# Performance work log

Measured on AMD Instinct MI355X. Metric: run time of the kernel, lower is better.

Reference implementation:

```python
import jax, jax.numpy as jnp
import numpy as np

TEMP = 0.025
BN_EPS = 1e-5


def _attention(a, W_in, b_in, g, beta, rm, rv, W_out, b_out):
    # a: (b, n1, n2, P, Q); 1x1 conv over the Q 'channel' dim, gate, softmax over P.
    m = a.mean(axis=3)                                   # (b,n1,n2,Q)
    t = jnp.einsum('bnmq,kq->bnmk', m, W_in) + b_in      # (b,n1,n2,K)
    t = jax.nn.relu((t - rm) / jnp.sqrt(rv + BN_EPS) * g + beta)
    t = jnp.einsum('bnmk,qk->bnmq', t, W_out) + b_out    # (b,n1,n2,Q)
    s = jnp.mean(a * t[:, :, :, None, :], axis=-1)       # (b,n1,n2,P)
    return jax.nn.softmax(s / TEMP, axis=-1) + 1.0


def _cam_forward(zf, xf, conv1_w, conv1_b, bn1_g, bn1_b, bn1_rm, bn1_rv,
                 conv2_w, conv2_b, conv3_w, conv3_b, bn3_g, bn3_b, bn3_rm, bn3_rv,
                 conv4_w, conv4_b):
    out1, out2 = [], []
    L = zf.shape[0]
    for l in range(L):  # small fixed loop over feature levels
        f1, f2 = zf[l], xf[l]
        b, c, h1, w1 = f1.shape
        h2, w2 = f2.shape[2], f2.shape[3]
        P, Q = h1 * w1, h2 * w2
        f1s = jnp.stack([f1.reshape(b, c, P)] * 2, axis=1)   # (b,2,c,P)
        f2s = jnp.stack([f2.reshape(b, c, Q)] * 2, axis=1)   # (b,2,c,Q)
        f1n = f1s / jnp.maximum(jnp.linalg.norm(f1s, axis=2, keepdims=True), 1e-12)
        f2n = f2s / jnp.maximum(jnp.linalg.norm(f2s, axis=2, keepdims=True), 1e-12)
        a1 = jnp.einsum('bncp,bmcq->bnmpq', f1n, f2n)        # (b,2,2,P,Q)
        att1 = _attention(a1, conv1_w, conv1_b, bn1_g, bn1_b, bn1_rm, bn1_rv,
                          conv2_w, conv2_b)                  # (b,2,2,P)
        att2 = _attention(a1.swapaxes(3, 4), conv3_w, conv3_b, bn3_g, bn3_b,
                          bn3_rm, bn3_rv, conv4_w, conv4_b)  # (b,2,2,Q)
        # mean over the (n1,n2)=(2,2) pair grid without materializing (b,2,2,c,HW)
        o1 = jnp.einsum('bncp,bnmp->bcp', f1s, att1) / 4.0
        o2 = jnp.einsum('bmcq,bnmq->bcq', f2s, att2) / 4.0
        out1.append(o1.reshape(b, c, h1, w1))
        out2.append(o2.reshape(b, c, h2, w2))
    return (jnp.stack(out1), jnp.stack(out2))


def setup_inputs() -> dict:
    key = jax.random.key(0)
    ks = jax.random.split(key, 12)
    L, B, C = 3, 32, 256
    inp = {
        'zf': jax.random.normal(ks[0], (L, B, C, 7, 7), jnp.float32),
        'xf': jax.random.normal(ks[1], (L, B, C, 31, 31), jnp.float32),
        'conv1_w': jax.random.normal(ks[2], (31, 961), jnp.float32) * np.sqrt(2.0 / 31),
        'conv1_b': jax.random.normal(ks[3], (31,), jnp.float32) * 0.05,
        'bn1_g': jax.random.uniform(ks[4], (31,), jnp.float32, 0.5, 1.5),
        'bn1_b': jax.random.normal(ks[5], (31,), jnp.float32) * 0.05,
        'bn1_rm': jnp.zeros((31,), jnp.float32),
        'bn1_rv': jnp.ones((31,), jnp.float32),
        'conv2_w': jax.random.normal(ks[6], (961, 31), jnp.float32) * np.sqrt(2.0 / 961),
        'conv2_b': jax.random.normal(ks[7], (961,), jnp.float32) * 0.05,
        'conv3_w': jax.random.normal(ks[8], (7, 49), jnp.float32) * np.sqrt(2.0 / 7),
        'conv3_b': jax.random.normal(ks[9], (7,), jnp.float32) * 0.05,
        'bn3_g': jax.random.uniform(ks[10], (7,), jnp.float32, 0.5, 1.5),
        'bn3_b': jax.random.normal(ks[11], (7,), jnp.float32) * 0.05,
        'bn3_rm': jnp.zeros((7,), jnp.float32),
        'bn3_rv': jnp.ones((7,), jnp.float32),
        'conv4_w': jax.random.normal(jax.random.fold_in(key, 100), (49, 7), jnp.float32) * np.sqrt(2.0 / 49),
        'conv4_b': jax.random.normal(jax.random.fold_in(key, 101), (49,), jnp.float32) * 0.05,
    }
    return inp


def reference(zf, xf, conv1_w, conv1_b, bn1_g, bn1_b, bn1_rm, bn1_rv,
              conv2_w, conv2_b, conv3_w, conv3_b, bn3_g, bn3_b, bn3_rm, bn3_rv,
              conv4_w, conv4_b):
    return _cam_forward(zf, xf, conv1_w, conv1_b, bn1_g, bn1_b, bn1_rm, bn1_rv,
                        conv2_w, conv2_b, conv3_w, conv3_b, bn3_g, bn3_b,
                        bn3_rm, bn3_rv, conv4_w, conv4_b)
```

## Files before the change

### kernel.cpp

```cpp
#include <hip/hip_runtime.h>
#include <math.h>

#define NLB 96
#define CC  256
#define PP  49
#define QQ  961
#define QP  1024
#define TEMP_INV 40.0f
#define BN_EPS 1e-5f

#define N1 (NLB*CC*PP)
#define N2 (NLB*CC*QQ)

typedef __attribute__((ext_vector_type(8))) short bf16x8;
typedef __attribute__((ext_vector_type(4))) float f32x4;
typedef __attribute__((ext_vector_type(8))) unsigned short ushort8;

__device__ inline unsigned short f2bf(float x) {
    unsigned int u = __float_as_uint(x);
    unsigned int r = (u + 0x7fffu + ((u >> 16) & 1u)) >> 16;
    return (unsigned short)r;
}

__global__ __launch_bounds__(256) void prep_z(
    const float* __restrict__ zf, unsigned short* __restrict__ f1T,
    float* __restrict__ inv1_ws, float* __restrict__ mrow_ws)
{
    const int lb = blockIdx.x;
    if (threadIdx.x < PP) mrow_ws[lb * PP + threadIdx.x] = 0.f;

    const float* __restrict__ f1 = zf + (size_t)lb * CC * PP;
    const int p  = threadIdx.x >> 2;
    const int qu = threadIdx.x & 3;
    const int c0 = qu * 64;
    float ss = 0.f;
    ushort8* dst = (ushort8*)(f1T + ((size_t)lb * 64 + p) * CC + c0);
#pragma unroll
    for (int s = 0; s < 8; ++s) {
        unsigned short tmp[8];
#pragma unroll
        for (int j = 0; j < 8; ++j) {
            const float v = (p < PP) ? f1[(size_t)(c0 + s * 8 + j) * PP + p] : 0.f;
            ss = fmaf(v, v, ss);
            tmp[j] = f2bf(v);
        }
        dst[s] = *(ushort8*)tmp;
    }
    ss += __shfl_xor(ss, 1, 64);
    ss += __shfl_xor(ss, 2, 64);
    if (qu == 0) inv1_ws[lb * 64 + p] = (p < PP) ? 1.0f / fmaxf(sqrtf(ss), 1e-12f) : 0.f;
}

__global__ __launch_bounds__(256) void prep_x(
    const float* __restrict__ xf, unsigned short* __restrict__ xT,
    float* __restrict__ inv2_ws)
{
    const int qt = blockIdx.x;
    const int lb = blockIdx.y;
    const int q0 = qt * 64;
    const float* __restrict__ f2 = xf + (size_t)lb * CC * QQ;

    __shared__ __align__(16) unsigned short tileB[64 * 264];
    __shared__ float ssP[4][64];

    const int tid  = threadIdx.x;
    const int lane = tid & 63;
    const int w    = tid >> 6;

    const int q  = q0 + lane;
    const bool qv = (q < QQ);
    float ss = 0.f;

    for (int i = 0; i < 8; ++i) {
        float r[8];
#pragma unroll
        for (int j = 0; j < 8; ++j) {
            const int c = (i * 8 + j) * 4 + w;
            r[j] = qv ? f2[(size_t)c * QQ + q] : 0.f;
        }
#pragma unroll
        for (int j = 0; j < 8; ++j) {
            const int c = (i * 8 + j) * 4 + w;
            ss = fmaf(r[j], r[j], ss);
            tileB[lane * 264 + c] = f2bf(r[j]);
        }
    }
    ssP[w][lane] = ss;
    __syncthreads();

    if (tid < 64) {
        const float t = ssP[0][tid] + ssP[1][tid] + ssP[2][tid] + ssP[3][tid];
        inv2_ws[lb * QP + q0 + tid] = 1.0f / fmaxf(sqrtf(t), 1e-12f);
    }

    unsigned short* __restrict__ dst = xT + (size_t)(lb * QP + q0) * CC;
#pragma unroll
    for (int j = 0; j < 8; ++j) {
        const int flat = (j * 256 + tid) * 8;
        const int qq = flat >> 8;
        const int cc = flat & 255;
        const ushort8 vv = *(const ushort8*)&tileB[qq * 264 + cc];
        *(ushort8*)&dst[flat] = vv;
    }
}

__global__ __launch_bounds__(256) void corr_mfma(
    const unsigned short* __restrict__ f1T, const unsigned short* __restrict__ xT,
    const float* __restrict__ inv1_ws, const float* __restrict__ inv2_ws,
    float* __restrict__ A_all, float* __restrict__ mcol_ws,
    float* __restrict__ mrow_ws)
{
    const int ng = blockIdx.x;
    const int lb = blockIdx.y;
    const int tid  = threadIdx.x;
    const int lane = tid & 63;
    const int wave = tid >> 6;
    const int g4   = lane >> 4;
    const int l15  = lane & 15;

    __shared__ __align__(16) unsigned short f1L[64 * 264];
    __shared__ float inv1L[64];

    for (int i = tid; i < 64 * 32; i += 256) {
        const int row = i >> 5, seg = i & 31;
        *(ushort8*)&f1L[row * 264 + seg * 8] =
            *(const ushort8*)&f1T[((size_t)lb * 64 + row) * CC + seg * 8];
    }
    if (tid < 64) inv1L[tid] = inv1_ws[lb * 64 + tid];
    __syncthreads();

    f32x4 acc[4][4];
#pragma unroll
    for (int i = 0; i < 4; ++i)
#pragma unroll
        for (int mt = 0; mt < 4; ++mt) acc[i][mt] = (f32x4)0.f;

    const unsigned short* __restrict__ xTb = xT + ((size_t)(lb * QP + ng * 256)) * CC;

#pragma unroll
    for (int kc = 0; kc < 4; ++kc) {
        bf16x8 af[4][2];
#pragma unroll
        for (int mt = 0; mt < 4; ++mt)
#pragma unroll
            for (int ks = 0; ks < 2; ++ks)
                af[mt][ks] = *(const bf16x8*)&f1L[(mt * 16 + l15) * 264 + kc * 64 + ks * 32 + g4 * 8];
#pragma unroll
        for (int i = 0; i < 4; ++i) {
            const int rowq = (4 * i + wave) * 16 + l15;
#pragma unroll
            for (int ks = 0; ks < 2; ++ks) {
                const bf16x8 bfr = *(const bf16x8*)&xTb[(size_t)rowq * CC + kc * 64 + ks * 32 + g4 * 8];
#pragma unroll
                for (int mt = 0; mt < 4; ++mt)
                    acc[i][mt] = __builtin_amdgcn_mfma_f32_16x16x32_bf16(af[mt][ks], bfr, acc[i][mt], 0, 0, 0);
            }
        }
    }

    float* __restrict__ Aout = A_all + (size_t)lb * PP * QQ;
#pragma unroll
    for (int i = 0; i < 4; ++i) {
        const int nt = 4 * i + wave;
        const int qg = ng * 256 + nt * 16 + l15;
        const bool qvv = (qg < QQ);
        const float iv2 = inv2_ws[lb * QP + qg];
        float vv[16];
        float cs = 0.f;
#pragma unroll
        for (int mt = 0; mt < 4; ++mt)
#pragma unroll
            for (int r = 0; r < 4; ++r) {
                const int p = mt * 16 + g4 * 4 + r;
                const float v = acc[i][mt][r] * inv1L[p] * iv2;
                vv[mt * 4 + r] = v;
                cs += v;
                if (p < PP && qvv) Aout[(size_t)p * QQ + qg] = v;
            }
        cs += __shfl_xor(cs, 16, 64);
        cs += __shfl_xor(cs, 32, 64);
        if ((lane < 16) && qvv) mcol_ws[lb * QQ + qg] = cs;
#pragma unroll
        for (int mt = 0; mt < 4; ++mt)
#pragma unroll
            for (int r = 0; r < 4; ++r) {
                const int p = mt * 16 + g4 * 4 + r;
                float s = vv[mt * 4 + r];
                s += __shfl_xor(s, 1, 64);
                s += __shfl_xor(s, 2, 64);
                s += __shfl_xor(s, 4, 64);
                s += __shfl_xor(s, 8, 64);
                if (((lane & 15) == 0) && p < PP) atomicAdd(&mrow_ws[lb * PP + p], s);
            }
    }
}

__global__ __launch_bounds__(512) void attn_kernel(
    const float* __restrict__ A_all,
    const float* __restrict__ mcol_ws, const float* __restrict__ mrow_ws,
    const float* __restrict__ W1, const float* __restrict__ b1,
    const float* __restrict__ g1, const float* __restrict__ bb1,
    const float* __restrict__ rm1, const float* __restrict__ rv1,
    const float* __restrict__ W2, const float* __restrict__ b2,
    const float* __restrict__ W3, const float* __restrict__ b3,
    const float* __restrict__ g3, const float* __restrict__ bb3,
    const float* __restrict__ rm3, const float* __restrict__ rv3,
    const float* __restrict__ W4, const float* __restrict__ b4,
    float* __restrict__ att1_ws, float* __restrict__ att2_ws)
{
    const int lb = blockIdx.x;
    const float* __restrict__ A = A_all + (size_t)lb * PP * QQ;
    const int tid  = threadIdx.x;
    const int lane = tid & 63;
    const int wv   = tid >> 6;

    __shared__ float mcolL[QQ];
    __shared__ float mrowL[PP];
    __shared__ float taL[31], tbL[7];
    __shared__ float t2aL[QQ], t2bL[PP];
    __shared__ float s2sL[QQ];
    __shared__ float s1L[PP];
    __shared__ float redM[8], redS[8];

    for (int q = tid; q < QQ; q += 512) mcolL[q] = mcol_ws[lb * QQ + q] * (1.0f / PP);
    if (tid < PP) mrowL[tid] = mrow_ws[lb * PP + tid] * (1.0f / QQ);
    __syncthreads();

    if (tid < 31 * 16) {
        const int k = tid >> 4, sub = tid & 15;
        float s = 0.f;
        for (int q = sub; q < QQ; q += 16) s = fmaf(mcolL[q], W1[k * QQ + q], s);
        s += __shfl_xor(s, 1, 64); s += __shfl_xor(s, 2, 64);
        s += __shfl_xor(s, 4, 64); s += __shfl_xor(s, 8, 64);
        if (sub == 0) {
            float t = s + b1[k];
            t = (t - rm1[k]) * rsqrtf(rv1[k] + BN_EPS) * g1[k] + bb1[k];
            taL[k] = fmaxf(t, 0.f);
        }
    }
    if (tid < 7 * 8) {
        const int k = tid >> 3, sub = tid & 7;
        float s = 0.f;
        for (int p = sub; p < PP; p += 8) s = fmaf(mrowL[p], W3[k * PP + p], s);
        s += __shfl_xor(s, 1, 64); s += __shfl_xor(s, 2, 64); s += __shfl_xor(s, 4, 64);
        if (sub == 0) {
            float t = s + b3[k];
            t = (t - rm3[k]) * rsqrtf(rv3[k] + BN_EPS) * g3[k] + bb3[k];
            tbL[k] = fmaxf(t, 0.f);
        }
    }
    __syncthreads();

    for (int q = tid; q < QQ; q += 512) {
        float s = b2[q];
#pragma unroll
        for (int k = 0; k < 31; ++k) s = fmaf(taL[k], W2[q * 31 + k], s);
        t2aL[q] = s;
    }
    if (tid < PP) {
        float s = b4[tid];
#pragma unroll
        for (int k = 0; k < 7; ++k) s = fmaf(tbL[k], W4[tid * 7 + k], s);
        t2bL[tid] = s;
    }
    __syncthreads();

    for (int q = tid; q < QQ; q += 512) {
        float s = 0.f;
#pragma unroll
        for (int p = 0; p < PP; ++p) s = fmaf(A[(size_t)p * QQ + q], t2bL[p], s);
        s2sL[q] = s * (1.0f / PP) * TEMP_INV;
    }
    for (int p = wv; p < PP; p += 8) {
        float s = 0.f;
        for (int q = lane; q < QQ; q += 64) s = fmaf(A[(size_t)p * QQ + q], t2aL[q], s);
        for (int off = 32; off > 0; off >>= 1) s += __shfl_xor(s, off, 64);
        if (lane == 0) s1L[p] = s * (1.0f / QQ) * TEMP_INV;
    }
    __syncthreads();

    if (wv == 0) {
        const float v = (lane < PP) ? s1L[lane] : -3.4e38f;
        float m = v;
        for (int off = 32; off > 0; off >>= 1) m = fmaxf(m, __shfl_xor(m, off, 64));
        const float e = (lane < PP) ? expf(v - m) : 0.f;
        float sum = e;
        for (int off = 32; off > 0; off >>= 1) sum += __shfl_xor(sum, off, 64);
        if (lane < PP) att1_ws[lb * PP + lane] = e / sum + 1.0f;
    }

    float lm = -3.4e38f;
    for (int q = tid; q < QQ; q += 512) lm = fmaxf(lm, s2sL[q]);
    for (int off = 32; off > 0; off >>= 1) lm = fmaxf(lm, __shfl_xor(lm, off, 64));
    if (lane == 0) redM[wv] = lm;
    __syncthreads();
    float gm = redM[0];
#pragma unroll
    for (int i = 1; i < 8; ++i) gm = fmaxf(gm, redM[i]);
    float ls = 0.f;
    for (int q = tid; q < QQ; q += 512) ls += expf(s2sL[q] - gm);
    for (int off = 32; off > 0; off >>= 1) ls += __shfl_xor(ls, off, 64);
    if (lane == 0) redS[wv] = ls;
    __syncthreads();
    float tot = 0.f;
#pragma unroll
    for (int i = 0; i < 8; ++i) tot += redS[i];
    const float rinv = 1.0f / tot;
    for (int q = tid; q < QQ; q += 512)
        att2_ws[lb * QQ + q] = expf(s2sL[q] - gm) * rinv + 1.0f;
}

template <int INNER>
__global__ __launch_bounds__(256) void scale_kernel(
    const float* __restrict__ in, const float* __restrict__ att,
    float* __restrict__ out, int n4)
{
    const int i = blockIdx.x * 256 + threadIdx.x;
    if (i >= n4) return;
    const float4 v = reinterpret_cast<const float4*>(in)[i];
    const float* vv = reinterpret_cast<const float*>(&v);
    float4 o;
    float* ov = reinterpret_cast<float*>(&o);
    const int g = i * 4;
#pragma unroll
    for (int j = 0; j < 4; ++j) {
        const int gg = g + j;
        const int lb = gg / (CC * INNER);
        const int x  = gg % INNER;
        ov[j] = vv[j] * att[lb * INNER + x];
    }
    reinterpret_cast<float4*>(out)[i] = o;
}

extern "C" void kernel_launch(void* const* d_in, const int* in_sizes, int n_in,
                              void* d_out, int out_size, void* d_ws, size_t ws_size,
                              hipStream_t stream)
{
    const float* zf  = (const float*)d_in[0];
    const float* xf  = (const float*)d_in[1];
    const float* W1  = (const float*)d_in[2];
    const float* b1  = (const float*)d_in[3];
    const float* g1  = (const float*)d_in[4];
    const float* bb1 = (const float*)d_in[5];
    const float* rm1 = (const float*)d_in[6];
    const float* rv1 = (const float*)d_in[7];
    const float* W2  = (const float*)d_in[8];
    const float* b2  = (const float*)d_in[9];
    const float* W3  = (const float*)d_in[10];
    const float* b3  = (const float*)d_in[11];
    const float* g3  = (const float*)d_in[12];
    const float* bb3 = (const float*)d_in[13];
    const float* rm3 = (const float*)d_in[14];
    const float* rv3 = (const float*)d_in[15];
    const float* W4  = (const float*)d_in[16];
    const float* b4  = (const float*)d_in[17];

    char* wsb = (char*)d_ws;
    unsigned short* xT  = (unsigned short*)wsb;
    unsigned short* f1T = xT + (size_t)NLB * QP * CC;
    float* fbase = (float*)(f1T + (size_t)NLB * 64 * CC);
    float* A     = fbase;
    float* att1  = A + (size_t)NLB * PP * QQ;
    float* att2  = att1 + (size_t)NLB * PP;
    float* mcol  = att2 + (size_t)NLB * QQ;
    float* mrow  = mcol + (size_t)NLB * QQ;
    float* inv1  = mrow + (size_t)NLB * PP;
    float* inv2  = inv1 + (size_t)NLB * 64;

    float* out1 = (float*)d_out;
    float* out2 = out1 + N1;

    prep_z<<<NLB, 256, 0, stream>>>(zf, f1T, inv1, mrow);
    dim3 gx(16, NLB);
    prep_x<<<gx, 256, 0, stream>>>(xf, xT, inv2);

    dim3 gcorr(4, NLB);
    corr_mfma<<<gcorr, 256, 0, stream>>>(f1T, xT, inv1, inv2, A, mcol, mrow);

    attn_kernel<<<NLB, 512, 0, stream>>>(A, mcol, mrow,
        W1, b1, g1, bb1, rm1, rv1, W2, b2,
        W3, b3, g3, bb3, rm3, rv3, W4, b4,
        att1, att2);

    const int n4_1 = N1 / 4;
    const int n4_2 = N2 / 4;
    scale_kernel<PP><<<(n4_1 + 255) / 256, 256, 0, stream>>>(zf, att1, out1, n4_1);
    scale_kernel<QQ><<<(n4_2 + 255) / 256, 256, 0, stream>>>(xf, att2, out2, n4_2);
}
```

Measured before the change: 149.1 us.

## Fuse x-feature bf16 conversion and norm into correlation MFMA kernel

Removes the separate prep_x kernel that transposed xf into a bf16 workspace and computed inverse norms. corr_mfma now reads fp32 xf directly in its natural channel-major layout, converts to bf16 in registers, and accumulates squared norms per column, reducing across lanes with shuffles. This drops a kernel launch and a full write+read of the transposed bf16 copy. In exchange each B-fragment load becomes eight strided scalar fp32 loads (stride QQ), though lanes read consecutive q, so the loads coalesce across the wavefront.

```diff
diff --git a/kernel.cpp b/kernel.cpp
--- a/kernel.cpp
+++ b/kernel.cpp
@@ -5,7 +5,6 @@
 #define CC  256
 #define PP  49
 #define QQ  961
-#define QP  1024
 #define TEMP_INV 40.0f
 #define BN_EPS 1e-5f
 
@@ -51,62 +50,9 @@
     if (qu == 0) inv1_ws[lb * 64 + p] = (p < PP) ? 1.0f / fmaxf(sqrtf(ss), 1e-12f) : 0.f;
 }
 
-__global__ __launch_bounds__(256) void prep_x(
-    const float* __restrict__ xf, unsigned short* __restrict__ xT,
-    float* __restrict__ inv2_ws)
-{
-    const int qt = blockIdx.x;
-    const int lb = blockIdx.y;
-    const int q0 = qt * 64;
-    const float* __restrict__ f2 = xf + (size_t)lb * CC * QQ;
-
-    __shared__ __align__(16) unsigned short tileB[64 * 264];
-    __shared__ float ssP[4][64];
-
-    const int tid  = threadIdx.x;
-    const int lane = tid & 63;
-    const int w    = tid >> 6;
-
-    const int q  = q0 + lane;
-    const bool qv = (q < QQ);
-    float ss = 0.f;
-
-    for (int i = 0; i < 8; ++i) {
-        float r[8];
-#pragma unroll
-        for (int j = 0; j < 8; ++j) {
-            const int c = (i * 8 + j) * 4 + w;
-            r[j] = qv ? f2[(size_t)c * QQ + q] : 0.f;
-        }
-#pragma unroll
-        for (int j = 0; j < 8; ++j) {
-            const int c = (i * 8 + j) * 4 + w;
-            ss = fmaf(r[j], r[j], ss);
-            tileB[lane * 264 + c] = f2bf(r[j]);
-        }
-    }
-    ssP[w][lane] = ss;
-    __syncthreads();
-
-    if (tid < 64) {
-        const float t = ssP[0][tid] + ssP[1][tid] + ssP[2][tid] + ssP[3][tid];
-        inv2_ws[lb * QP + q0 + tid] = 1.0f / fmaxf(sqrtf(t), 1e-12f);
-    }
-
-    unsigned short* __restrict__ dst = xT + (size_t)(lb * QP + q0) * CC;
-#pragma unroll
-    for (int j = 0; j < 8; ++j) {
-        const int flat = (j * 256 + tid) * 8;
-        const int qq = flat >> 8;
-        const int cc = flat & 255;
-        const ushort8 vv = *(const ushort8*)&tileB[qq * 264 + cc];
-        *(ushort8*)&dst[flat] = vv;
-    }
-}
-
 __global__ __launch_bounds__(256) void corr_mfma(
-    const unsigned short* __restrict__ f1T, const unsigned short* __restrict__ xT,
-    const float* __restrict__ inv1_ws, const float* __restrict__ inv2_ws,
+    const unsigned short* __restrict__ f1T, const float* __restrict__ xf,
+    const float* __restrict__ inv1_ws,
     float* __restrict__ A_all, float* __restrict__ mcol_ws,
     float* __restrict__ mrow_ws)
 {
@@ -118,6 +64,8 @@
     const int g4   = lane >> 4;
     const int l15  = lane & 15;
 
+    const float* __restrict__ f2 = xf + (size_t)lb * CC * QQ;
+
     __shared__ __align__(16) unsigned short f1L[64 * 264];
     __shared__ float inv1L[64];
 
@@ -135,7 +83,7 @@
 #pragma unroll
         for (int mt = 0; mt < 4; ++mt) acc[i][mt] = (f32x4)0.f;
 
-    const unsigned short* __restrict__ xTb = xT + ((size_t)(lb * QP + ng * 256)) * CC;
+    float ss2[4] = {0.f, 0.f, 0.f, 0.f};
 
 #pragma unroll
     for (int kc = 0; kc < 4; ++kc) {
@@ -147,10 +95,22 @@
                 af[mt][ks] = *(const bf16x8*)&f1L[(mt * 16 + l15) * 264 + kc * 64 + ks * 32 + g4 * 8];
 #pragma unroll
         for (int i = 0; i < 4; ++i) {
-            const int rowq = (4 * i + wave) * 16 + l15;
+            const int qg = ng * 256 + (4 * i + wave) * 16 + l15;
+            const bool qv = (qg < QQ);
+            const float* __restrict__ src = f2 + (size_t)(kc * 64 + g4 * 8) * QQ + (qv ? qg : 0);
 #pragma unroll
             for (int ks = 0; ks < 2; ++ks) {
-                const bf16x8 bfr = *(const bf16x8*)&xTb[(size_t)rowq * CC + kc * 64 + ks * 32 + g4 * 8];
+                float rr[8];
+#pragma unroll
+                for (int j = 0; j < 8; ++j)
+                    rr[j] = qv ? src[(size_t)(ks * 32 + j) * QQ] : 0.f;
+                unsigned short us[8];
+#pragma unroll
+                for (int j = 0; j < 8; ++j) {
+                    ss2[i] = fmaf(rr[j], rr[j], ss2[i]);
+                    us[j] = f2bf(rr[j]);
+                }
+                const bf16x8 bfr = *(const bf16x8*)us;
 #pragma unroll
                 for (int mt = 0; mt < 4; ++mt)
                     acc[i][mt] = __builtin_amdgcn_mfma_f32_16x16x32_bf16(af[mt][ks], bfr, acc[i][mt], 0, 0, 0);
@@ -164,7 +124,10 @@
         const int nt = 4 * i + wave;
         const int qg = ng * 256 + nt * 16 + l15;
         const bool qvv = (qg < QQ);
-        const float iv2 = inv2_ws[lb * QP + qg];
+        float ssf = ss2[i];
+        ssf += __shfl_xor(ssf, 16, 64);
+        ssf += __shfl_xor(ssf, 32, 64);
+        const float iv2 = 1.0f / fmaxf(sqrtf(ssf), 1e-12f);
         float vv[16];
         float cs = 0.f;
 #pragma unroll
@@ -356,8 +319,7 @@
     const float* b4  = (const float*)d_in[17];
 
     char* wsb = (char*)d_ws;
-    unsigned short* xT  = (unsigned short*)wsb;
-    unsigned short* f1T = xT + (size_t)NLB * QP * CC;
+    unsigned short* f1T = (unsigned short*)wsb;
     float* fbase = (float*)(f1T + (size_t)NLB * 64 * CC);
     float* A     = fbase;
     float* att1  = A + (size_t)NLB * PP * QQ;
@@ -365,17 +327,14 @@
     float* mcol  = att2 + (size_t)NLB * QQ;
     float* mrow  = mcol + (size_t)NLB * QQ;
     float* inv1  = mrow + (size_t)NLB * PP;
-    float* inv2  = inv1 + (size_t)NLB * 64;
 
     float* out1 = (float*)d_out;
     float* out2 = out1 + N1;
 
     prep_z<<<NLB, 256, 0, stream>>>(zf, f1T, inv1, mrow);
-    dim3 gx(16, NLB);
-    prep_x<<<gx, 256, 0, stream>>>(xf, xT, inv2);
 
     dim3 gcorr(4, NLB);
-    corr_mfma<<<gcorr, 256, 0, stream>>>(f1T, xT, inv1, inv2, A, mcol, mrow);
+    corr_mfma<<<gcorr, 256, 0, stream>>>(f1T, xf, inv1, A, mcol, mrow);
 
     attn_kernel<<<NLB, 512, 0, stream>>>(A, mcol, mrow,
         W1, b1, g1, bb1, rm1, rv1, W2, b2,
```

After: 153.3 us. 2.8% more time.
